# Optimization experiments

Hardware: AMD Instinct MI355X
Metric: run time of the kernel (lower is better)

## Reference

```python
import jax, jax.numpy as jnp
import numpy as np

N, C, H, W = 4, 128, 64, 64
HEADS, KS, RED = 4, 7, 18
D = C // HEADS


def _layernorm(x, w, b, eps=1e-5):
    mu = x.mean(axis=-1, keepdims=True)
    var = ((x - mu) ** 2).mean(axis=-1, keepdims=True)
    return (x - mu) * jax.lax.rsqrt(var + eps) * w + b


def _gelu(x):
    return jax.nn.gelu(x, approximate=False)


def setup_inputs() -> dict:
    key = jax.random.key(0)
    ks = jax.random.split(key, 16)
    s = 0.02
    inp = {
        'x': jax.random.normal(ks[0], (N, C, H, W), jnp.float32),
        'ln1_w': jnp.ones((C,), jnp.float32), 'ln1_b': jnp.zeros((C,), jnp.float32),
        'ln2_w': jnp.ones((C,), jnp.float32), 'ln2_b': jnp.zeros((C,), jnp.float32),
        'qkv_w': jax.random.normal(ks[1], (C, 3 * C), jnp.float32) * s,
        'qkv_b': jnp.zeros((3 * C,), jnp.float32),
        'proj_w': jax.random.normal(ks[2], (C, C), jnp.float32) * s,
        'proj_b': jnp.zeros((C,), jnp.float32),
        'rpb': jax.random.normal(ks[3], (HEADS, 2 * KS - 1, 2 * KS - 1), jnp.float32) * s,
        'conv1_w': jax.random.normal(ks[4], (C, C // 4), jnp.float32) * s,
        'conv1_b': jnp.zeros((C // 4,), jnp.float32),
        'conv2_w': jax.random.normal(ks[5], (C // 4, C), jnp.float32) * s,
        'conv2_b': jnp.zeros((C,), jnp.float32),
        'ca1_w': jax.random.normal(ks[6], (C, C // RED), jnp.float32) * s,
        'ca1_b': jnp.zeros((C // RED,), jnp.float32),
        'ca2_w': jax.random.normal(ks[7], (C // RED, C), jnp.float32) * s,
        'ca2_b': jnp.zeros((C,), jnp.float32),
        'fc1_w': jax.random.normal(ks[8], (C, 4 * C), jnp.float32) * s,
        'fc1_b': jnp.zeros((4 * C,), jnp.float32),
        'fc2_w': jax.random.normal(ks[9], (4 * C, C), jnp.float32) * s,
        'fc2_b': jnp.zeros((C,), jnp.float32),
    }
    return inp


def _na2d(xc, qkv_w, qkv_b, rpb, proj_w, proj_b):
    # xc: [N, H, W, C] -> neighborhood attention with clamped k x k windows (NATTEN semantics)
    n, h, w, c = xc.shape
    qkv = (xc @ qkv_w + qkv_b).reshape(n, h, w, 3, HEADS, D)
    q, k, v = qkv[..., 0, :, :], qkv[..., 1, :, :], qkv[..., 2, :, :]
    q = q * (D ** -0.5)
    half = KS // 2
    ni = jnp.clip(jnp.arange(h) - half, 0, h - KS)          # window start per query row
    nj = jnp.clip(jnp.arange(w) - half, 0, w - KS)
    idx_i = ni[:, None] + jnp.arange(KS)                     # [H, KS]
    idx_j = nj[:, None] + jnp.arange(KS)                     # [W, KS]
    # gather key/value windows: [N, H, KS, W, KS, heads, D]
    kw = k[:, idx_i][:, :, :, idx_j]
    vw = v[:, idx_i][:, :, :, idx_j]
    attn = jnp.einsum('nijhd,niajbhd->nijhab', q, kw)        # [N,H,W,heads,KS,KS]
    bi = idx_i - jnp.arange(h)[:, None] + (KS - 1)           # rel-pos bias row index [H,KS]
    bj = idx_j - jnp.arange(w)[:, None] + (KS - 1)           # [W,KS]
    bias = rpb[:, bi][:, :, :, bj]                           # [heads,H,KS,W,KS]
    attn = attn + bias.transpose(1, 3, 0, 2, 4)[None]        # -> [1,H,W,heads,KS,KS]
    attn = jax.nn.softmax(attn.reshape(n, h, w, HEADS, KS * KS), axis=-1)
    attn = attn.reshape(n, h, w, HEADS, KS, KS)
    out = jnp.einsum('nijhab,niajbhd->nijhd', attn, vw).reshape(n, h, w, c)
    return out @ proj_w + proj_b


def reference(x, ln1_w, ln1_b, ln2_w, ln2_b, qkv_w, qkv_b, proj_w, proj_b, rpb,
              conv1_w, conv1_b, conv2_w, conv2_b, ca1_w, ca1_b, ca2_w, ca2_b,
              fc1_w, fc1_b, fc2_w, fc2_b):
    n, c, h, w = x.shape
    xs = x.transpose(0, 2, 3, 1).reshape(n, h * w, c)        # n (h w) c
    shortcut = xs
    xn = _layernorm(xs, ln1_w, ln1_b)
    xc = xn.reshape(n, h, w, c)
    # conv branch: 1x1 -> GELU -> 1x1 -> channel attention
    t = _gelu(xc @ conv1_w + conv1_b) @ conv2_w + conv2_b
    g = t.mean(axis=(1, 2))                                  # global avg pool [N,C]
    g = jax.nn.sigmoid(jax.nn.relu(g @ ca1_w + ca1_b) @ ca2_w + ca2_b)
    ca_x = (t * g[:, None, None, :]).reshape(n, h * w, c)
    # neighborhood attention branch
    na_x = _na2d(xc, qkv_w, qkv_b, rpb, proj_w, proj_b).reshape(n, h * w, c)
    x2 = shortcut + na_x + ca_x * 0.02
    m = _gelu(_layernorm(x2, ln2_w, ln2_b) @ fc1_w + fc1_b) @ fc2_w + fc2_b
    x3 = x2 + m
    return x3.reshape(n, h, w, c).transpose(0, 3, 1, 2)
```

## Files before the change

### kernel.cpp

```cpp
#include <hip/hip_runtime.h>
#include <hip/hip_bf16.h>
#include <math.h>

#define NB 4
#define CC 128
#define HH 64
#define WW 64
#define HEADS 4
#define KS 7
#define DD 32
#define HW 4096
#define MTOT 16384

typedef unsigned short BF;
typedef short short8 __attribute__((ext_vector_type(8)));
typedef float floatx4 __attribute__((ext_vector_type(4)));

__device__ __forceinline__ float gelu_f(float x) {
    return 0.5f * x * (1.0f + erff(x * 0.70710678118654752440f));
}

__device__ __forceinline__ BF f2bf(float f) {
    union { float f; unsigned u; } a; a.f = f;
    unsigned u = a.u;
    unsigned r = u + 0x7FFFu + ((u >> 16) & 1u);
    return (BF)(r >> 16);
}

__device__ __forceinline__ float bf2f(BF v) {
    return __uint_as_float(((unsigned)v) << 16);
}

#define LDK 40
#define LDK128 136

__global__ __launch_bounds__(256) void ln1t_kernel(
    const float* __restrict__ x, const float* __restrict__ w,
    const float* __restrict__ b, BF* __restrict__ out,
    float* __restrict__ part,
    const float* __restrict__ qkv_w, const float* __restrict__ conv1_w,
    const float* __restrict__ conv2_w, const float* __restrict__ proj_w,
    const float* __restrict__ fc1_w, const float* __restrict__ fc2_w,
    BF* __restrict__ qkvT, BF* __restrict__ c1T, BF* __restrict__ c2T,
    BF* __restrict__ projT2, BF* __restrict__ fc1T2, BF* __restrict__ fc2T2)
{
    const int blk = blockIdx.x;
    const int t  = threadIdx.x;

    if (blk >= 512) {
        for (int idx = (blk - 512) * 256 + t; idx < 204800; idx += 32768) {
            if (idx < 49152) {
                int l = idx, n = l >> 7, k = l & 127;
                qkvT[l] = f2bf(qkv_w[k * 384 + n]);
            } else if (idx < 53248) {
                int l = idx - 49152, n = l >> 7, k = l & 127;
                c1T[l] = f2bf(conv1_w[k * 32 + n]);
            } else if (idx < 57344) {
                int l = idx - 53248, n = l >> 5, k = l & 31;
                c2T[l] = f2bf(conv2_w[k * 128 + n]);
            } else if (idx < 73728) {
                int l = idx - 57344, kk = l & 31, n = (l >> 5) & 127, ks = l >> 12;
                projT2[l] = f2bf(proj_w[(ks * 32 + kk) * 128 + n]);
            } else if (idx < 139264) {
                int l = idx - 73728, kk = l & 31, n = (l >> 5) & 511, ks = l >> 14;
                fc1T2[l] = f2bf(fc1_w[(ks * 32 + kk) * 512 + n]);
            } else {
                int l = idx - 139264, kk = l & 31, n = (l >> 5) & 127, ks = l >> 12;
                fc2T2[l] = f2bf(fc2_w[(ks * 32 + kk) * 128 + n]);
            }
        }
        return;
    }

    __shared__ float xt[128][33];
    __shared__ float mus[32], rss[32];
    const int n  = blk >> 7;
    const int p0 = (blk & 127) * 32;
    if (blk < 4 && t < 128) part[blk * CC + t] = 0.f;

    {
        int pp = t & 31, c8 = t >> 5;
        #pragma unroll 4
        for (int it = 0; it < 16; it++) {
            int c = it * 8 + c8;
            xt[c][pp] = x[(size_t)(n * CC + c) * HW + p0 + pp];
        }
    }
    __syncthreads();
    {
        int pp2 = t >> 3, cb = t & 7;
        float s = 0.f;
        #pragma unroll
        for (int u = 0; u < 16; u++) s += xt[cb + u * 8][pp2];
        s += __shfl_xor(s, 1); s += __shfl_xor(s, 2); s += __shfl_xor(s, 4);
        float mu = s * (1.0f / CC);
        float v = 0.f;
        #pragma unroll
        for (int u = 0; u < 16; u++) { float d = xt[cb + u * 8][pp2] - mu; v += d * d; }
        v += __shfl_xor(v, 1); v += __shfl_xor(v, 2); v += __shfl_xor(v, 4);
        if (cb == 0) { mus[pp2] = mu; rss[pp2] = rsqrtf(v * (1.0f / CC) + 1e-5f); }
    }
    __syncthreads();
    {
        #pragma unroll
        for (int it = 0; it < 2; it++) {
            int pp2 = (t >> 4) + it * 16;
            int c0  = (t & 15) * 8;
            float mu = mus[pp2], rs = rss[pp2];
            int m = n * HW + p0 + pp2;
            short8 o;
            #pragma unroll
            for (int u = 0; u < 8; u++)
                o[u] = (short)f2bf((xt[c0 + u][pp2] - mu) * rs * w[c0 + u] + b[c0 + u]);
            *(short8*)(out + (size_t)m * CC + c0) = o;
        }
    }
}

__global__ __launch_bounds__(256) void phase2(
    const BF* __restrict__ xn, const BF* __restrict__ qkvT,
    const float* __restrict__ qkv_b, BF* __restrict__ qkv_out,
    const BF* __restrict__ c1T, const float* __restrict__ b1,
    const BF* __restrict__ c2T, const float* __restrict__ b2,
    BF* __restrict__ tout, float* __restrict__ part)
{
    __shared__ __align__(16) char smem[26624];
    const int bid = blockIdx.x;
    const int t = threadIdx.x;
    const int w = t >> 6, lane = t & 63, q = lane >> 4, r16 = lane & 15;

    if (bid < 768) {
        BF* Bl = (BF*)smem;
        const int col0 = (bid % 6) * 64;
        const int row0 = (bid / 6) * 128;
        {
            int nn = t >> 2;
            int kk = (t & 3) * 32;
            const BF* src = qkvT + (size_t)(col0 + nn) * 128 + kk;
            #pragma unroll
            for (int u = 0; u < 4; u++)
                *(uint4*)(Bl + nn * LDK128 + kk + u * 8) = *(const uint4*)(src + u * 8);
        }
        __syncthreads();
        #pragma unroll
        for (int half = 0; half < 2; half++) {
            floatx4 acc[4] = {};
            const BF* arow = xn + (size_t)(row0 + half * 64 + w * 16 + r16) * CC;
            #pragma unroll
            for (int ks = 0; ks < 4; ks++) {
                short8 af = *(const short8*)(arow + ks * 32 + q * 8);
                #pragma unroll
                for (int nt = 0; nt < 4; nt++) {
                    short8 bf = *(const short8*)(Bl + (nt * 16 + r16) * LDK128 + ks * 32 + q * 8);
                    acc[nt] = __builtin_amdgcn_mfma_f32_16x16x32_bf16(af, bf, acc[nt], 0, 0, 0);
                }
            }
            #pragma unroll
            for (int nt = 0; nt < 4; nt++) {
                int col = col0 + nt * 16 + r16;
                float bv = qkv_b[col];
                #pragma unroll
                for (int reg = 0; reg < 4; reg++) {
                    int row = row0 + half * 64 + w * 16 + q * 4 + reg;
                    qkv_out[(size_t)row * 384 + col] = f2bf(acc[nt][reg] + bv);
                }
            }
        }
        return;
    }
    BF*    W1l = (BF*)smem;
    BF*    W2l = (BF*)(smem + 8704);
    BF*    Hl  = (BF*)(smem + 18944);
    float* red = (float*)(smem + 24064);
    const int row0 = (bid - 768) * 64;
    {
        #pragma unroll
        for (int it = 0; it < 2; it++) {
            int idx = it * 256 + t;
            int nn = idx >> 4, u = idx & 15;
            *(uint4*)(W1l + nn * LDK128 + u * 8) = *(const uint4*)(c1T + nn * 128 + u * 8);
        }
    }
    {
        #pragma unroll
        for (int it = 0; it < 2; it++) {
            int idx = it * 256 + t;
            int nn = idx >> 2, u = idx & 3;
            *(uint4*)(W2l + nn * LDK + u * 8) = *(const uint4*)(c2T + nn * 32 + u * 8);
        }
    }
    __syncthreads();
    floatx4 a1[2] = {};
    const BF* arow = xn + (size_t)(row0 + w * 16 + r16) * CC;
    #pragma unroll
    for (int ks = 0; ks < 4; ks++) {
        short8 af = *(const short8*)(arow + ks * 32 + q * 8);
        #pragma unroll
        for (int nt = 0; nt < 2; nt++) {
            short8 bf = *(const short8*)(W1l + (nt * 16 + r16) * LDK128 + ks * 32 + q * 8);
            a1[nt] = __builtin_amdgcn_mfma_f32_16x16x32_bf16(af, bf, a1[nt], 0, 0, 0);
        }
    }
    #pragma unroll
    for (int nt = 0; nt < 2; nt++) {
        int col = nt * 16 + r16;
        float bv = b1[col];
        #pragma unroll
        for (int reg = 0; reg < 4; reg++)
            Hl[(w * 16 + q * 4 + reg) * LDK + col] = f2bf(gelu_f(a1[nt][reg] + bv));
    }
    __syncthreads();
    floatx4 a2[8] = {};
    short8 af2 = *(const short8*)(Hl + (w * 16 + r16) * LDK + q * 8);
    #pragma unroll
    for (int nt = 0; nt < 8; nt++) {
        short8 bf = *(const short8*)(W2l + (nt * 16 + r16) * LDK + q * 8);
        a2[nt] = __builtin_amdgcn_mfma_f32_16x16x32_bf16(af2, bf, a2[nt], 0, 0, 0);
    }
    #pragma unroll
    for (int nt = 0; nt < 8; nt++) {
        int col = nt * 16 + r16;
        float bv = b2[col];
        float s = 0.f;
        #pragma unroll
        for (int reg = 0; reg < 4; reg++) {
            int row = row0 + w * 16 + q * 4 + reg;
            float v = a2[nt][reg] + bv;
            tout[(size_t)row * CC + col] = f2bf(v);
            s += v;
        }
        s += __shfl_xor(s, 16);
        s += __shfl_xor(s, 32);
        if (lane < 16) red[w * 128 + col] = s;
    }
    __syncthreads();
    if (t < 128) {
        float cs = red[t] + red[128 + t] + red[256 + t] + red[384 + t];
        atomicAdd(&part[(row0 >> 12) * CC + t], cs);
    }
}

__global__ __launch_bounds__(256) void na_mfma_kernel(
    const BF* __restrict__ qkv, const float* __restrict__ rpb,
    BF* __restrict__ outp,
    const float* __restrict__ part,
    const float* __restrict__ ca1_w, const float* __restrict__ ca1_b,
    const float* __restrict__ ca2_w, const float* __restrict__ ca2_b,
    float* __restrict__ glw)
{
    __shared__ __align__(16) BF Kt[224][40];
    __shared__ __align__(16) BF Vt[32][232];
    __shared__ __align__(16) BF Qb[64][40];
    __shared__ __align__(16) BF Pl[4][16][232];
    __shared__ float rb[169];

    const int b = blockIdx.x;
    const int t = threadIdx.x;

    if (b == 1024) {
        float* gsm = (float*)Kt;
        float* h1s = (float*)Qb;
        if (t < 128) {
            #pragma unroll
            for (int nn = 0; nn < 4; nn++)
                gsm[nn * 128 + t] = part[nn * CC + t] * (1.0f / HW);
        }
        __syncthreads();
        if (t < 224) {
            int pair = t >> 3, s = t & 7;
            int nn = pair / 7, r = pair % 7;
            float a = 0.f;
            #pragma unroll
            for (int k = 0; k < 16; k++)
                a += gsm[nn * 128 + s + k * 8] * ca1_w[(s + k * 8) * 7 + r];
            a += __shfl_xor(a, 1); a += __shfl_xor(a, 2); a += __shfl_xor(a, 4);
            if (s == 0) h1s[pair] = fmaxf(a + ca1_b[r], 0.f);
        }
        __syncthreads();
        if (t < 128) {
            #pragma unroll
            for (int nn = 0; nn < 4; nn++) {
                float o = ca2_b[t];
                #pragma unroll
                for (int r = 0; r < 7; r++) o += h1s[nn * 7 + r] * ca2_w[r * 128 + t];
                glw[nn * CC + t] = 1.0f / (1.0f + expf(-o));
            }
        }
        return;
    }

    const int h = b & 3;
    const int tile = b >> 2;
    const int n = tile >> 6;
    const int ti = (tile >> 3) & 7, tj = tile & 7;
    const int w = t >> 6, lane = t & 63, quad = lane >> 4, r16 = lane & 15;
    const int i0 = ti * 8, j0 = tj * 8;
    const int wi0 = max(i0 - 3, 0), wj0 = max(j0 - 3, 0);
    const int R  = min(wi0 + 13, 63) - wi0 + 1;
    const int Rj = min(wj0 + 13, 63) - wj0 + 1;

    for (int idx = t; idx < 896; idx += 256) {
        int key = idx >> 2, ch = idx & 3;
        int kr = key >> 4, kc = key & 15;
        uint4 v = {0u, 0u, 0u, 0u};
        if (kr < R && kc < Rj) {
            size_t pix = (size_t)((n * HH + wi0 + kr) * WW + wj0 + kc);
            v = *(const uint4*)(qkv + pix * 384 + 128 + h * DD + ch * 8);
        }
        *(uint4*)&Kt[key][ch * 8] = v;
    }
    for (int idx = t; idx < 896; idx += 256) {
        int key = idx >> 2, ch = idx & 3;
        int kr = key >> 4, kc = key & 15;
        if (kr < R && kc < Rj) {
            size_t pix = (size_t)((n * HH + wi0 + kr) * WW + wj0 + kc);
            uint4 v = *(const uint4*)(qkv + pix * 384 + 256 + h * DD + ch * 8);
            const BF* pv = (const BF*)&v;
            #pragma unroll
            for (int u = 0; u < 8; u++) Vt[ch * 8 + u][key] = pv[u];
        } else {
            #pragma unroll
            for (int u = 0; u < 8; u++) Vt[ch * 8 + u][key] = 0;
        }
    }
    {
        int q = t >> 2, ch = t & 3;
        size_t mq = (size_t)((n * HH + i0 + (q >> 3)) * WW + j0 + (q & 7));
        *(uint4*)&Qb[q][ch * 8] = *(const uint4*)(qkv + mq * 384 + h * DD + ch * 8);
    }
    if (t < 169) rb[t] = rpb[h * 169 + t];
    __syncthreads();

    const int kt0 = min(max(i0 + 2 * w - 3, 0), HH - KS) - wi0;

    int oi[4], cok[4], bj0[4], ai_[4];
    #pragma unroll
    for (int reg = 0; reg < 4; reg++) {
        int q = w * 16 + quad * 4 + reg;
        int i = i0 + (q >> 3), j = j0 + (q & 7);
        int ni = min(max(i - 3, 0), HH - KS), nj = min(max(j - 3, 0), WW - KS);
        oi[reg]  = ni - wi0;
        ai_[reg] = ni - i + 6;
        int dc = r16 - (nj - wj0);
        cok[reg] = ((unsigned)dc < 7u) ? 1 : 0;
        bj0[reg] = min(max(dc + (nj - j + 6), 0), 12);
    }

    short8 aq = *(const short8*)&Qb[w * 16 + r16][quad * 8];
    floatx4 S[8];
    #pragma unroll
    for (int jt = 0; jt < 8; jt++) {
        floatx4 z = {0.f, 0.f, 0.f, 0.f};
        short8 bk = *(const short8*)&Kt[(kt0 + jt) * 16 + r16][quad * 8];
        S[jt] = __builtin_amdgcn_mfma_f32_16x16x32_bf16(aq, bk, z, 0, 0, 0);
    }
    const float scale = 0.17677669529663688110f;
    #pragma unroll
    for (int jt = 0; jt < 8; jt++) {
        #pragma unroll
        for (int reg = 0; reg < 4; reg++) {
            int dr = kt0 + jt - oi[reg];
            bool ok = ((unsigned)dr < 7u) && cok[reg];
            int bi = min(max(dr + ai_[reg], 0), 12);
            float bias = rb[bi * 13 + bj0[reg]];
            S[jt][reg] = ok ? fmaf(S[jt][reg], scale, bias) : -1e30f;
        }
    }
    float rinv[4];
    #pragma unroll
    for (int reg = 0; reg < 4; reg++) {
        float m = S[0][reg];
        #pragma unroll
        for (int jt = 1; jt < 8; jt++) m = fmaxf(m, S[jt][reg]);
        m = fmaxf(m, __shfl_xor(m, 1));
        m = fmaxf(m, __shfl_xor(m, 2));
        m = fmaxf(m, __shfl_xor(m, 4));
        m = fmaxf(m, __shfl_xor(m, 8));
        float s = 0.f;
        #pragma unroll
        for (int jt = 0; jt < 8; jt++) {
            float e = __expf(S[jt][reg] - m);
            S[jt][reg] = e;
            s += e;
        }
        s += __shfl_xor(s, 1);
        s += __shfl_xor(s, 2);
        s += __shfl_xor(s, 4);
        s += __shfl_xor(s, 8);
        rinv[reg] = 1.0f / s;
    }
    #pragma unroll
    for (int jt = 0; jt < 8; jt++)
        #pragma unroll
        for (int reg = 0; reg < 4; reg++)
            Pl[w][quad * 4 + reg][(kt0 + jt) * 16 + r16] = f2bf(S[jt][reg] * rinv[reg]);
    if (kt0 & 1) {
        #pragma unroll
        for (int reg = 0; reg < 4; reg++) {
            Pl[w][quad * 4 + reg][(kt0 - 1) * 16 + r16] = 0;
            Pl[w][quad * 4 + reg][(kt0 + 8) * 16 + r16] = 0;
        }
    }

    const int ks0 = kt0 >> 1;
    const int nch = 4 + (kt0 & 1);
    floatx4 O0 = {0.f, 0.f, 0.f, 0.f}, O1 = {0.f, 0.f, 0.f, 0.f};
    #pragma unroll
    for (int c2 = 0; c2 < 5; c2++) {
        if (c2 < nch) {
            int ks = ks0 + c2;
            short8 ap = *(const short8*)&Pl[w][r16][ks * 32 + quad * 8];
            short8 b0 = *(const short8*)&Vt[r16][ks * 32 + quad * 8];
            short8 b1 = *(const short8*)&Vt[16 + r16][ks * 32 + quad * 8];
            O0 = __builtin_amdgcn_mfma_f32_16x16x32_bf16(ap, b0, O0, 0, 0, 0);
            O1 = __builtin_amdgcn_mfma_f32_16x16x32_bf16(ap, b1, O1, 0, 0, 0);
        }
    }
    #pragma unroll
    for (int reg = 0; reg < 4; reg++) {
        int q = w * 16 + quad * 4 + reg;
        size_t m = (size_t)((n * HH + i0 + (q >> 3)) * WW + j0 + (q & 7));
        outp[m * CC + h * DD + r16]      = f2bf(O0[reg]);
        outp[m * CC + h * DD + 16 + r16] = f2bf(O1[reg]);
    }
}

__global__ __launch_bounds__(512, 6) void tail_kernel(
    const BF* __restrict__ A, const BF* __restrict__ projT2,
    const float* __restrict__ proj_b, const float* __restrict__ x,
    const BF* __restrict__ tbuf, const float* __restrict__ glw,
    const float* __restrict__ w2, const float* __restrict__ b2,
    const BF* __restrict__ fc1T2, const float* __restrict__ fc1_b,
    const BF* __restrict__ fc2T2, const float* __restrict__ fc2_b,
    float* __restrict__ out)
{
    __shared__ __align__(16) char sarena[9216];
    __shared__ __align__(16) BF ln2l[16][136];
    __shared__ __align__(16) BF hl[16][520];
    __shared__ float gl[128];
    __shared__ float S1[8][16], S2[8][16];

    float* xs = (float*)sarena;
    float* st = (float*)sarena;

    const int t = threadIdx.x;
    const int w = t >> 6, lane = t & 63, quad = lane >> 4, r16 = lane & 15;
    const int row0 = blockIdx.x * 16;
    const int n = row0 >> 12, p0 = row0 & 4095;
    const int col = w * 16 + r16;

    {
        int p4 = t & 3, c = t >> 2;
        float4 v = *(const float4*)(x + (size_t)(n * CC + c) * HW + p0 + p4 * 4);
        xs[(p4 * 4 + 0) * 132 + c] = v.x; xs[(p4 * 4 + 1) * 132 + c] = v.y;
        xs[(p4 * 4 + 2) * 132 + c] = v.z; xs[(p4 * 4 + 3) * 132 + c] = v.w;
    }
    if (t < 128) gl[t] = glw[n * CC + t];

    float gv  = glw[n * CC + col];
    float pbv = proj_b[col];
    float tvr[4];
    #pragma unroll
    for (int reg = 0; reg < 4; reg++) {
        int lr = quad * 4 + reg;
        tvr[reg] = bf2f(tbuf[(size_t)(row0 + lr) * CC + col]);
    }

    floatx4 acc = {};
    const BF* arow = A + (size_t)(row0 + r16) * CC;
    #pragma unroll
    for (int ks = 0; ks < 4; ks++) {
        short8 af = *(const short8*)(arow + ks * 32 + quad * 8);
        short8 bf = *(const short8*)(projT2 + ((size_t)(ks * 128 + col)) * 32 + quad * 8);
        acc = __builtin_amdgcn_mfma_f32_16x16x32_bf16(af, bf, acc, 0, 0, 0);
    }
    __syncthreads();

    float x2r[4];
    float s1[4], s2[4];
    #pragma unroll
    for (int reg = 0; reg < 4; reg++) {
        int lr = quad * 4 + reg;
        float v = acc[reg] + pbv + xs[lr * 132 + col] + 0.02f * tvr[reg] * gv;
        x2r[reg] = v;
        s1[reg] = v; s2[reg] = v * v;
    }
    #pragma unroll
    for (int reg = 0; reg < 4; reg++) {
        #pragma unroll
        for (int off = 1; off < 16; off <<= 1) {
            s1[reg] += __shfl_xor(s1[reg], off);
            s2[reg] += __shfl_xor(s2[reg], off);
        }
    }
    if (r16 == 0) {
        #pragma unroll
        for (int reg = 0; reg < 4; reg++) {
            S1[w][quad * 4 + reg] = s1[reg];
            S2[w][quad * 4 + reg] = s2[reg];
        }
    }
    __syncthreads();
    float mu[4], rr[4];
    #pragma unroll
    for (int reg = 0; reg < 4; reg++) {
        int r = quad * 4 + reg;
        float t1 = 0.f, t2 = 0.f;
        #pragma unroll
        for (int ww = 0; ww < 8; ww++) { t1 += S1[ww][r]; t2 += S2[ww][r]; }
        mu[reg] = t1 * (1.0f / CC);
        float var = t2 * (1.0f / CC) - mu[reg] * mu[reg];
        rr[reg] = rsqrtf(var + 1e-5f);
    }
    {
        float wv = w2[col], bv2 = b2[col];
        #pragma unroll
        for (int reg = 0; reg < 4; reg++) {
            int lr = quad * 4 + reg;
            ln2l[lr][col] = f2bf((x2r[reg] - mu[reg]) * rr[reg] * wv + bv2);
        }
    }
    __syncthreads();

    short8 af1[4];
    #pragma unroll
    for (int ks = 0; ks < 4; ks++)
        af1[ks] = *(const short8*)&ln2l[r16][ks * 32 + quad * 8];
    floatx4 a2[4] = {};
    #pragma unroll
    for (int ks = 0; ks < 4; ks++) {
        #pragma unroll
        for (int nt = 0; nt < 4; nt++) {
            int c1col = w * 64 + nt * 16 + r16;
            short8 bf = *(const short8*)(fc1T2 + ((size_t)(ks * 512 + c1col)) * 32 + quad * 8);
            a2[nt] = __builtin_amdgcn_mfma_f32_16x16x32_bf16(af1[ks], bf, a2[nt], 0, 0, 0);
        }
    }
    #pragma unroll
    for (int nt = 0; nt < 4; nt++) {
        int c1col = w * 64 + nt * 16 + r16;
        float bv = fc1_b[c1col];
        #pragma unroll
        for (int reg = 0; reg < 4; reg++) {
            int lr = quad * 4 + reg;
            hl[lr][c1col] = f2bf(gelu_f(a2[nt][reg] + bv));
        }
    }
    __syncthreads();

    floatx4 a3 = {};
    #pragma unroll
    for (int ks = 0; ks < 16; ks++) {
        short8 af = *(const short8*)&hl[r16][ks * 32 + quad * 8];
        short8 bf = *(const short8*)(fc2T2 + ((size_t)(ks * 128 + col)) * 32 + quad * 8);
        a3 = __builtin_amdgcn_mfma_f32_16x16x32_bf16(af, bf, a3, 0, 0, 0);
    }
    {
        float bv = fc2_b[col];
        #pragma unroll
        for (int reg = 0; reg < 4; reg++) {
            int lr = quad * 4 + reg;
            st[col * 18 + lr] = a3[reg] + bv + x2r[reg];
        }
    }
    __syncthreads();
    {
        int c = t >> 2, u4 = t & 3;
        float4 v;
        v.x = st[c * 18 + u4 * 4 + 0];
        v.y = st[c * 18 + u4 * 4 + 1];
        v.z = st[c * 18 + u4 * 4 + 2];
        v.w = st[c * 18 + u4 * 4 + 3];
        *(float4*)(out + (size_t)(n * CC + c) * HW + p0 + u4 * 4) = v;
    }
}

extern "C" void kernel_launch(void* const* d_in, const int* in_sizes, int n_in,
                              void* d_out, int out_size, void* d_ws, size_t ws_size,
                              hipStream_t stream)
{
    const float* x       = (const float*)d_in[0];
    const float* ln1_w   = (const float*)d_in[1];
    const float* ln1_b   = (const float*)d_in[2];
    const float* ln2_w   = (const float*)d_in[3];
    const float* ln2_b   = (const float*)d_in[4];
    const float* qkv_w   = (const float*)d_in[5];
    const float* qkv_b   = (const float*)d_in[6];
    const float* proj_w  = (const float*)d_in[7];
    const float* proj_b  = (const float*)d_in[8];
    const float* rpb     = (const float*)d_in[9];
    const float* conv1_w = (const float*)d_in[10];
    const float* conv1_b = (const float*)d_in[11];
    const float* conv2_w = (const float*)d_in[12];
    const float* conv2_b = (const float*)d_in[13];
    const float* ca1_w   = (const float*)d_in[14];
    const float* ca1_b   = (const float*)d_in[15];
    const float* ca2_w   = (const float*)d_in[16];
    const float* ca2_b   = (const float*)d_in[17];
    const float* fc1_w   = (const float*)d_in[18];
    const float* fc1_b   = (const float*)d_in[19];
    const float* fc2_w   = (const float*)d_in[20];
    const float* fc2_b   = (const float*)d_in[21];
    float* out = (float*)d_out;

    char* ws = (char*)d_ws;
    BF*    xn_bf   = (BF*)(ws);
    BF*    qkv_bf  = (BF*)(ws + 4194304);
    BF*    t_bf    = (BF*)(ws + 16777216);
    BF*    na_bf   = (BF*)(ws + 20971520);
    float* part    = (float*)(ws + 25165824);
    BF*    qkvT    = (BF*)(ws + 25167872);
    BF*    c1T     = (BF*)(ws + 25266176);
    BF*    c2T     = (BF*)(ws + 25274368);
    BF*    projT2  = (BF*)(ws + 25282560);
    BF*    fc1T2   = (BF*)(ws + 25315328);
    BF*    fc2T2   = (BF*)(ws + 25446400);
    float* glw     = (float*)(ws + 25577472);

    ln1t_kernel<<<640, 256, 0, stream>>>(x, ln1_w, ln1_b, xn_bf, part,
        qkv_w, conv1_w, conv2_w, proj_w, fc1_w, fc2_w,
        qkvT, c1T, c2T, projT2, fc1T2, fc2T2);
    phase2<<<1024, 256, 0, stream>>>(xn_bf, qkvT, qkv_b, qkv_bf,
                                     c1T, conv1_b, c2T, conv2_b, t_bf, part);
    na_mfma_kernel<<<1025, 256, 0, stream>>>(qkv_bf, rpb, na_bf,
                                             part, ca1_w, ca1_b, ca2_w, ca2_b, glw);
    tail_kernel<<<1024, 512, 0, stream>>>(na_bf, projT2, proj_b, x, t_bf, glw,
                                          ln2_w, ln2_b, fc1T2, fc1_b,
                                          fc2T2, fc2_b, out);
}
```

Before: 159.9 us.

## Fuse LayerNorm1 with QKV and conv-branch GEMMs into one front kernel

LayerNorm1 is fused with the QKV projection and the conv1/GELU/conv2 branch in a single kernel, so the normalized activations stay in shared memory and registers instead of being written to and re-read from global memory. The weight transpose and bf16 conversion move into a separate small prep kernel that also zeroes the pooling accumulators. The front kernel reads B fragments straight from global or L2 rather than staging them in LDS, and its grid drops to 512 blocks. That lowers parallelism per launch and adds redundant weight loads across blocks.

```diff
diff --git a/kernel.cpp b/kernel.cpp
--- a/kernel.cpp
+++ b/kernel.cpp
@@ -32,51 +32,62 @@
 }
 
 #define LDK 40
-#define LDK128 136
-
-__global__ __launch_bounds__(256) void ln1t_kernel(
-    const float* __restrict__ x, const float* __restrict__ w,
-    const float* __restrict__ b, BF* __restrict__ out,
-    float* __restrict__ part,
+
+__global__ __launch_bounds__(256) void prep_kernel(
     const float* __restrict__ qkv_w, const float* __restrict__ conv1_w,
     const float* __restrict__ conv2_w, const float* __restrict__ proj_w,
     const float* __restrict__ fc1_w, const float* __restrict__ fc2_w,
     BF* __restrict__ qkvT, BF* __restrict__ c1T, BF* __restrict__ c2T,
-    BF* __restrict__ projT2, BF* __restrict__ fc1T2, BF* __restrict__ fc2T2)
+    BF* __restrict__ projT2, BF* __restrict__ fc1T2, BF* __restrict__ fc2T2,
+    float* __restrict__ part)
 {
     const int blk = blockIdx.x;
-    const int t  = threadIdx.x;
-
-    if (blk >= 512) {
-        for (int idx = (blk - 512) * 256 + t; idx < 204800; idx += 32768) {
-            if (idx < 49152) {
-                int l = idx, n = l >> 7, k = l & 127;
-                qkvT[l] = f2bf(qkv_w[k * 384 + n]);
-            } else if (idx < 53248) {
-                int l = idx - 49152, n = l >> 7, k = l & 127;
-                c1T[l] = f2bf(conv1_w[k * 32 + n]);
-            } else if (idx < 57344) {
-                int l = idx - 53248, n = l >> 5, k = l & 31;
-                c2T[l] = f2bf(conv2_w[k * 128 + n]);
-            } else if (idx < 73728) {
-                int l = idx - 57344, kk = l & 31, n = (l >> 5) & 127, ks = l >> 12;
-                projT2[l] = f2bf(proj_w[(ks * 32 + kk) * 128 + n]);
-            } else if (idx < 139264) {
-                int l = idx - 73728, kk = l & 31, n = (l >> 5) & 511, ks = l >> 14;
-                fc1T2[l] = f2bf(fc1_w[(ks * 32 + kk) * 512 + n]);
-            } else {
-                int l = idx - 139264, kk = l & 31, n = (l >> 5) & 127, ks = l >> 12;
-                fc2T2[l] = f2bf(fc2_w[(ks * 32 + kk) * 128 + n]);
-            }
-        }
-        return;
-    }
-
+    const int t = threadIdx.x;
+    if (blk == 0 && t < 512) part[t] = 0.f;
+    for (int idx = blk * 256 + t; idx < 204800; idx += 32768) {
+        if (idx < 49152) {
+            int l = idx, n = l >> 7, k = l & 127;
+            qkvT[l] = f2bf(qkv_w[k * 384 + n]);
+        } else if (idx < 53248) {
+            int l = idx - 49152, n = l >> 7, k = l & 127;
+            c1T[l] = f2bf(conv1_w[k * 32 + n]);
+        } else if (idx < 57344) {
+            int l = idx - 53248, n = l >> 5, k = l & 31;
+            c2T[l] = f2bf(conv2_w[k * 128 + n]);
+        } else if (idx < 73728) {
+            int l = idx - 57344, kk = l & 31, n = (l >> 5) & 127, ks = l >> 12;
+            projT2[l] = f2bf(proj_w[(ks * 32 + kk) * 128 + n]);
+        } else if (idx < 139264) {
+            int l = idx - 73728, kk = l & 31, n = (l >> 5) & 511, ks = l >> 14;
+            fc1T2[l] = f2bf(fc1_w[(ks * 32 + kk) * 512 + n]);
+        } else {
+            int l = idx - 139264, kk = l & 31, n = (l >> 5) & 127, ks = l >> 12;
+            fc2T2[l] = f2bf(fc2_w[(ks * 32 + kk) * 128 + n]);
+        }
+    }
+}
+
+__global__ __launch_bounds__(256) void front_kernel(
+    const float* __restrict__ x, const float* __restrict__ lnw,
+    const float* __restrict__ lnb,
+    const BF* __restrict__ qkvT, const float* __restrict__ qkv_b,
+    BF* __restrict__ qkv_out,
+    const BF* __restrict__ c1T, const float* __restrict__ b1,
+    const BF* __restrict__ c2T, const float* __restrict__ b2,
+    BF* __restrict__ tout, float* __restrict__ part)
+{
     __shared__ float xt[128][33];
     __shared__ float mus[32], rss[32];
-    const int n  = blk >> 7;
+    __shared__ __align__(16) BF xnl[32][136];
+    __shared__ __align__(16) BF Hl[32][LDK];
+    __shared__ float red[2][128];
+
+    const int blk = blockIdx.x;
+    const int t = threadIdx.x;
+    const int n = blk >> 7;
     const int p0 = (blk & 127) * 32;
-    if (blk < 4 && t < 128) part[blk * CC + t] = 0.f;
+    const int base = n * HW + p0;
+    const int w = t >> 6, lane = t & 63, q = lane >> 4, r16 = lane & 15;
 
     {
         int pp = t & 31, c8 = t >> 5;
@@ -107,136 +118,81 @@
             int pp2 = (t >> 4) + it * 16;
             int c0  = (t & 15) * 8;
             float mu = mus[pp2], rs = rss[pp2];
-            int m = n * HW + p0 + pp2;
             short8 o;
             #pragma unroll
             for (int u = 0; u < 8; u++)
-                o[u] = (short)f2bf((xt[c0 + u][pp2] - mu) * rs * w[c0 + u] + b[c0 + u]);
-            *(short8*)(out + (size_t)m * CC + c0) = o;
-        }
-    }
-}
-
-__global__ __launch_bounds__(256) void phase2(
-    const BF* __restrict__ xn, const BF* __restrict__ qkvT,
-    const float* __restrict__ qkv_b, BF* __restrict__ qkv_out,
-    const BF* __restrict__ c1T, const float* __restrict__ b1,
-    const BF* __restrict__ c2T, const float* __restrict__ b2,
-    BF* __restrict__ tout, float* __restrict__ part)
-{
-    __shared__ __align__(16) char smem[26624];
-    const int bid = blockIdx.x;
-    const int t = threadIdx.x;
-    const int w = t >> 6, lane = t & 63, q = lane >> 4, r16 = lane & 15;
-
-    if (bid < 768) {
-        BF* Bl = (BF*)smem;
-        const int col0 = (bid % 6) * 64;
-        const int row0 = (bid / 6) * 128;
-        {
-            int nn = t >> 2;
-            int kk = (t & 3) * 32;
-            const BF* src = qkvT + (size_t)(col0 + nn) * 128 + kk;
-            #pragma unroll
-            for (int u = 0; u < 4; u++)
-                *(uint4*)(Bl + nn * LDK128 + kk + u * 8) = *(const uint4*)(src + u * 8);
-        }
-        __syncthreads();
-        #pragma unroll
-        for (int half = 0; half < 2; half++) {
-            floatx4 acc[4] = {};
-            const BF* arow = xn + (size_t)(row0 + half * 64 + w * 16 + r16) * CC;
-            #pragma unroll
-            for (int ks = 0; ks < 4; ks++) {
-                short8 af = *(const short8*)(arow + ks * 32 + q * 8);
-                #pragma unroll
-                for (int nt = 0; nt < 4; nt++) {
-                    short8 bf = *(const short8*)(Bl + (nt * 16 + r16) * LDK128 + ks * 32 + q * 8);
-                    acc[nt] = __builtin_amdgcn_mfma_f32_16x16x32_bf16(af, bf, acc[nt], 0, 0, 0);
-                }
+                o[u] = (short)f2bf((xt[c0 + u][pp2] - mu) * rs * lnw[c0 + u] + lnb[c0 + u]);
+            *(short8*)&xnl[pp2][c0] = o;
+        }
+    }
+    __syncthreads();
+
+    const int rt = w & 1, whi = w >> 1;
+
+    short8 axn[4];
+    #pragma unroll
+    for (int ks = 0; ks < 4; ks++)
+        axn[ks] = *(const short8*)&xnl[rt * 16 + r16][ks * 32 + q * 8];
+
+    {
+        floatx4 a1 = {};
+        #pragma unroll
+        for (int ks = 0; ks < 4; ks++) {
+            short8 bf = *(const short8*)(c1T + (size_t)(whi * 16 + r16) * 128 + ks * 32 + q * 8);
+            a1 = __builtin_amdgcn_mfma_f32_16x16x32_bf16(axn[ks], bf, a1, 0, 0, 0);
+        }
+        int col = whi * 16 + r16;
+        float bv = b1[col];
+        #pragma unroll
+        for (int reg = 0; reg < 4; reg++)
+            Hl[rt * 16 + q * 4 + reg][col] = f2bf(gelu_f(a1[reg] + bv));
+    }
+    __syncthreads();
+
+    {
+        short8 af2 = *(const short8*)&Hl[rt * 16 + r16][q * 8];
+        floatx4 a2[4] = {};
+        #pragma unroll
+        for (int nt = 0; nt < 4; nt++) {
+            int col = whi * 64 + nt * 16 + r16;
+            short8 bf = *(const short8*)(c2T + (size_t)col * 32 + q * 8);
+            a2[nt] = __builtin_amdgcn_mfma_f32_16x16x32_bf16(af2, bf, a2[nt], 0, 0, 0);
+        }
+        #pragma unroll
+        for (int nt = 0; nt < 4; nt++) {
+            int col = whi * 64 + nt * 16 + r16;
+            float bv = b2[col];
+            float s = 0.f;
+            #pragma unroll
+            for (int reg = 0; reg < 4; reg++) {
+                int row = base + rt * 16 + q * 4 + reg;
+                float v = a2[nt][reg] + bv;
+                tout[(size_t)row * CC + col] = f2bf(v);
+                s += v;
             }
-            #pragma unroll
-            for (int nt = 0; nt < 4; nt++) {
-                int col = col0 + nt * 16 + r16;
-                float bv = qkv_b[col];
-                #pragma unroll
-                for (int reg = 0; reg < 4; reg++) {
-                    int row = row0 + half * 64 + w * 16 + q * 4 + reg;
-                    qkv_out[(size_t)row * 384 + col] = f2bf(acc[nt][reg] + bv);
-                }
-            }
-        }
-        return;
-    }
-    BF*    W1l = (BF*)smem;
-    BF*    W2l = (BF*)(smem + 8704);
-    BF*    Hl  = (BF*)(smem + 18944);
-    float* red = (float*)(smem + 24064);
-    const int row0 = (bid - 768) * 64;
-    {
-        #pragma unroll
-        for (int it = 0; it < 2; it++) {
-            int idx = it * 256 + t;
-            int nn = idx >> 4, u = idx & 15;
-            *(uint4*)(W1l + nn * LDK128 + u * 8) = *(const uint4*)(c1T + nn * 128 + u * 8);
-        }
-    }
-    {
-        #pragma unroll
-        for (int it = 0; it < 2; it++) {
-            int idx = it * 256 + t;
-            int nn = idx >> 2, u = idx & 3;
-            *(uint4*)(W2l + nn * LDK + u * 8) = *(const uint4*)(c2T + nn * 32 + u * 8);
-        }
-    }
-    __syncthreads();
-    floatx4 a1[2] = {};
-    const BF* arow = xn + (size_t)(row0 + w * 16 + r16) * CC;
-    #pragma unroll
-    for (int ks = 0; ks < 4; ks++) {
-        short8 af = *(const short8*)(arow + ks * 32 + q * 8);
-        #pragma unroll
-        for (int nt = 0; nt < 2; nt++) {
-            short8 bf = *(const short8*)(W1l + (nt * 16 + r16) * LDK128 + ks * 32 + q * 8);
-            a1[nt] = __builtin_amdgcn_mfma_f32_16x16x32_bf16(af, bf, a1[nt], 0, 0, 0);
-        }
-    }
-    #pragma unroll
-    for (int nt = 0; nt < 2; nt++) {
-        int col = nt * 16 + r16;
-        float bv = b1[col];
-        #pragma unroll
-        for (int reg = 0; reg < 4; reg++)
-            Hl[(w * 16 + q * 4 + reg) * LDK + col] = f2bf(gelu_f(a1[nt][reg] + bv));
-    }
-    __syncthreads();
-    floatx4 a2[8] = {};
-    short8 af2 = *(const short8*)(Hl + (w * 16 + r16) * LDK + q * 8);
-    #pragma unroll
-    for (int nt = 0; nt < 8; nt++) {
-        short8 bf = *(const short8*)(W2l + (nt * 16 + r16) * LDK + q * 8);
-        a2[nt] = __builtin_amdgcn_mfma_f32_16x16x32_bf16(af2, bf, a2[nt], 0, 0, 0);
-    }
-    #pragma unroll
-    for (int nt = 0; nt < 8; nt++) {
-        int col = nt * 16 + r16;
-        float bv = b2[col];
-        float s = 0.f;
-        #pragma unroll
-        for (int reg = 0; reg < 4; reg++) {
-            int row = row0 + w * 16 + q * 4 + reg;
-            float v = a2[nt][reg] + bv;
-            tout[(size_t)row * CC + col] = f2bf(v);
-            s += v;
-        }
-        s += __shfl_xor(s, 16);
-        s += __shfl_xor(s, 32);
-        if (lane < 16) red[w * 128 + col] = s;
-    }
-    __syncthreads();
-    if (t < 128) {
-        float cs = red[t] + red[128 + t] + red[256 + t] + red[384 + t];
-        atomicAdd(&part[(row0 >> 12) * CC + t], cs);
+            s += __shfl_xor(s, 16);
+            s += __shfl_xor(s, 32);
+            if (lane < 16) red[rt][whi * 64 + nt * 16 + lane] = s;
+        }
+    }
+    __syncthreads();
+    if (t < 128) atomicAdd(&part[n * CC + t], red[0][t] + red[1][t]);
+
+    #pragma unroll
+    for (int nt = 0; nt < 12; nt++) {
+        int col = whi * 16 + nt * 32 + r16;
+        floatx4 acc = {};
+        #pragma unroll
+        for (int ks = 0; ks < 4; ks++) {
+            short8 bf = *(const short8*)(qkvT + (size_t)col * 128 + ks * 32 + q * 8);
+            acc = __builtin_amdgcn_mfma_f32_16x16x32_bf16(axn[ks], bf, acc, 0, 0, 0);
+        }
+        float bv = qkv_b[col];
+        #pragma unroll
+        for (int reg = 0; reg < 4; reg++) {
+            int row = base + rt * 16 + q * 4 + reg;
+            qkv_out[(size_t)row * 384 + col] = f2bf(acc[reg] + bv);
+        }
     }
 }
 
@@ -604,7 +560,6 @@
     float* out = (float*)d_out;
 
     char* ws = (char*)d_ws;
-    BF*    xn_bf   = (BF*)(ws);
     BF*    qkv_bf  = (BF*)(ws + 4194304);
     BF*    t_bf    = (BF*)(ws + 16777216);
     BF*    na_bf   = (BF*)(ws + 20971520);
@@ -617,11 +572,11 @@
     BF*    fc2T2   = (BF*)(ws + 25446400);
     float* glw     = (float*)(ws + 25577472);
 
-    ln1t_kernel<<<640, 256, 0, stream>>>(x, ln1_w, ln1_b, xn_bf, part,
-        qkv_w, conv1_w, conv2_w, proj_w, fc1_w, fc2_w,
-        qkvT, c1T, c2T, projT2, fc1T2, fc2T2);
-    phase2<<<1024, 256, 0, stream>>>(xn_bf, qkvT, qkv_b, qkv_bf,
-                                     c1T, conv1_b, c2T, conv2_b, t_bf, part);
+    prep_kernel<<<128, 256, 0, stream>>>(qkv_w, conv1_w, conv2_w, proj_w,
+                                         fc1_w, fc2_w, qkvT, c1T, c2T,
+                                         projT2, fc1T2, fc2T2, part);
+    front_kernel<<<512, 256, 0, stream>>>(x, ln1_w, ln1_b, qkvT, qkv_b, qkv_bf,
+                                          c1T, conv1_b, c2T, conv2_b, t_bf, part);
     na_mfma_kernel<<<1025, 256, 0, stream>>>(qkv_bf, rpb, na_bf,
                                              part, ca1_w, ca1_b, ca2_w, ca2_b, glw);
     tail_kernel<<<1024, 512, 0, stream>>>(na_bf, projT2, proj_b, x, t_bf, glw,
```

Measured after the change: 166.9 us. 4.4% more time.
